# Kernel optimization log

Measured on AMD Instinct MI355X. Metric: run time of the kernel, lower is better.

## Reference

```python
import jax, jax.numpy as jnp
import numpy as np

B, S, D = 2, 2048, 1024
H, HKV, DK = 16, 4, 64          # n_heads, n_kv_heads, head dim
NREP = H // HKV                  # 4


def apply_rope(x):
    # Faithful to the original: positions run over x.shape[-2], which is the
    # HEAD axis (x is [B, S, H, DK]) due to how the torch module is written.
    d = x.shape[-1]
    h = x.shape[-2]
    inv_freq = 1.0 / (10000.0 ** (jnp.arange(0, d, 2, dtype=jnp.float32) / d))
    freqs = jnp.arange(h, dtype=jnp.float32)[:, None] * inv_freq[None, :]  # [H, DK/2]
    cos, sin = jnp.cos(freqs), jnp.sin(freqs)
    x1, x2 = x[..., 0::2], x[..., 1::2]
    # interleave back: stack on new last axis then flatten
    return jnp.stack([x1 * cos - x2 * sin, x1 * sin + x2 * cos], axis=-1).reshape(x.shape)


def setup_inputs() -> dict:
    key = jax.random.key(0)
    kx, kq, kk, kv, ko = jax.random.split(key, 5)
    std = 0.02
    x = jax.random.normal(kx, (B, S, D), jnp.float32)
    w_q = jax.random.normal(kq, (D, H * DK), jnp.float32) * std
    w_k = jax.random.normal(kk, (D, HKV * DK), jnp.float32) * std
    w_v = jax.random.normal(kv, (D, HKV * DK), jnp.float32) * std
    w_o = jax.random.normal(ko, (D, D), jnp.float32) * std
    # causal mask, broadcastable to [B, H, S, S]
    mask = jnp.tril(jnp.ones((S, S), bool))[None, None]  # [1,1,S,S]
    return {"x": x, "w_q": w_q, "w_k": w_k, "w_v": w_v, "w_o": w_o, "mask": mask}


def reference(x, w_q, w_k, w_v, w_o, mask):
    b, s, d = x.shape
    Q = (x @ w_q).reshape(b, s, H, DK)
    K = (x @ w_k).reshape(b, s, HKV, DK)
    V = (x @ w_v).reshape(b, s, HKV, DK)
    Q = apply_rope(Q)
    K = apply_rope(K)
    # [B,H,S,DK] with query heads grouped per kv head (matches repeat_interleave)
    Q = Q.transpose(0, 2, 1, 3).reshape(b, HKV, NREP, s, DK)
    K = K.transpose(0, 2, 1, 3)  # [B,HKV,S,DK]
    V = V.transpose(0, 2, 1, 3)
    scores = jnp.einsum('bgrqd,bgkd->bgrqk', Q, K) / np.float32(np.sqrt(DK))
    scores = scores.astype(jnp.float32)
    neg = jnp.finfo(jnp.float32).min
    scores = jnp.where(mask[:, :, None, :, :], scores, neg)  # [1,1,1,S,S] broadcast
    w = jax.nn.softmax(scores, axis=-1)
    ctx = jnp.einsum('bgrqk,bgkd->bgrqd', w, V)  # [B,HKV,NREP,S,DK]
    ctx = ctx.reshape(b, H, s, DK).transpose(0, 2, 1, 3).reshape(b, s, d)
    return ctx @ w_o
```

## Files before the change

### kernel.cpp

```cpp
#include <hip/hip_runtime.h>
#include <hip/hip_bf16.h>

#define S_LEN 2048
#define NBATCH 2
#define DMODEL 1024
#define NHEAD 16
#define NKV 4
#define HDIM 64

typedef __attribute__((ext_vector_type(4))) float f32x4;
typedef __attribute__((ext_vector_type(8))) short s16x8;

#define QSCALE 0.18033688011112042f

__device__ __forceinline__ unsigned short f32_bf16(float f) {
    unsigned int u = __float_as_uint(f);
    u += 0x7FFFu + ((u >> 16) & 1u);
    return (unsigned short)(u >> 16);
}

__device__ __forceinline__ unsigned int cvt_pk_bf16(float a, float b) {
    unsigned int r;
    asm("v_cvt_pk_bf16_f32 %0, %1, %2" : "=v"(r) : "v"(a), "v"(b));
    return r;
}

__device__ __forceinline__ void cvtT_body(const float* __restrict__ in,
                                          unsigned short* __restrict__ out,
                                          int N, int n_off, int bx, int by, int tid) {
    __shared__ float t[64][65];
    const int n0 = bx * 64;
    const int k0 = by * 64;
    const int r  = tid >> 4;
    const int c4 = (tid & 15) * 4;
    #pragma unroll
    for (int i = 0; i < 4; ++i) {
        const float4 v = *reinterpret_cast<const float4*>(
            in + (size_t)(k0 + i*16 + r) * N + n0 + c4);
        t[i*16 + r][c4+0] = v.x; t[i*16 + r][c4+1] = v.y;
        t[i*16 + r][c4+2] = v.z; t[i*16 + r][c4+3] = v.w;
    }
    __syncthreads();
    #pragma unroll
    for (int i = 0; i < 4; ++i) {
        const int n = i*16 + r;
        ushort4 o;
        o.x = f32_bf16(t[c4+0][n]); o.y = f32_bf16(t[c4+1][n]);
        o.z = f32_bf16(t[c4+2][n]); o.w = f32_bf16(t[c4+3][n]);
        *reinterpret_cast<ushort4*>(out + (size_t)(n_off + n0 + n) * 1024 + k0 + c4) = o;
    }
}

__global__ __launch_bounds__(256) void cvt_all_k(
    const float* __restrict__ x,  const float* __restrict__ wq,
    const float* __restrict__ wk, const float* __restrict__ wv,
    const float* __restrict__ wo,
    unsigned short* __restrict__ xb, unsigned short* __restrict__ Wqkvt,
    unsigned short* __restrict__ Wot)
{
    const int bid = blockIdx.x;
    if (bid < 4096) {
        const int i = bid * 256 + threadIdx.x;
        const float4 v = reinterpret_cast<const float4*>(x)[i];
        ushort4 r;
        r.x = f32_bf16(v.x); r.y = f32_bf16(v.y);
        r.z = f32_bf16(v.z); r.w = f32_bf16(v.w);
        reinterpret_cast<ushort4*>(xb)[i] = r;
    } else if (bid < 4480) {
        const int t  = bid - 4096;
        int bx = t % 24;
        const int by = t / 24;
        const float* in; int N, n_off;
        if (bx < 16)      { in = wq; N = 1024; n_off = 0; }
        else if (bx < 20) { in = wk; N = 256;  n_off = 1024; bx -= 16; }
        else              { in = wv; N = 256;  n_off = 1280; bx -= 20; }
        cvtT_body(in, Wqkvt, N, n_off, bx, by, threadIdx.x);
    } else {
        const int t = bid - 4480;
        cvtT_body(wo, Wot, 1024, 0, t % 16, t / 16, threadIdx.x);
    }
}

using gas_u32 = const unsigned int __attribute__((address_space(1))) *;
using las_u32 = unsigned int __attribute__((address_space(3))) *;

template<int EPI>
__global__ __launch_bounds__(256, 3) void gemm2_k(
    const unsigned short* __restrict__ A,
    const unsigned short* __restrict__ Bt,
    int N, int K,
    float* __restrict__ OutF,
    unsigned short* __restrict__ Qb,
    unsigned short* __restrict__ Kbuf,
    unsigned short* __restrict__ Vbuf)
{
    __shared__ unsigned short As[2][128 * 64];
    __shared__ unsigned short Bs[2][64 * 64];

    const int tid  = threadIdx.x;
    const int lane = tid & 63;
    const int l15  = lane & 15;
    const int l4   = lane >> 4;
    const int wave = tid >> 6;
    const int wm   = wave >> 1;
    const int wn   = wave & 1;
    const int bm   = blockIdx.y * 128;
    const int bn   = blockIdx.x * 64;

    f32x4 acc[4][2] = {};

    const int NT = K >> 6;

    #define GSTAGE(buf, k0)                                                        \
        {                                                                          \
            _Pragma("unroll")                                                      \
            for (int p = 0; p < 4; ++p) {                                          \
                const int c = p*256 + tid, r_ = c >> 3;                            \
                const int nc = (c & 7) ^ (r_ & 7);                                 \
                __builtin_amdgcn_global_load_lds(                                  \
                    (gas_u32)(A + (size_t)(bm + r_) * K + (k0) + nc*8),            \
                    (las_u32)(&As[buf][c*8]), 16, 0, 0);                           \
            }                                                                      \
            _Pragma("unroll")                                                      \
            for (int p = 0; p < 2; ++p) {                                          \
                const int c = p*256 + tid, r_ = c >> 3;                            \
                const int nc = (c & 7) ^ (r_ & 7);                                 \
                __builtin_amdgcn_global_load_lds(                                  \
                    (gas_u32)(Bt + (size_t)(bn + r_) * K + (k0) + nc*8),           \
                    (las_u32)(&Bs[buf][c*8]), 16, 0, 0);                           \
            }                                                                      \
        }

    GSTAGE(0, 0); __syncthreads();

    for (int kt = 0; kt < NT; ++kt) {
        const int cur = kt & 1;
        if (kt + 1 < NT) GSTAGE(cur ^ 1, (kt + 1) << 6);
        #pragma unroll
        for (int ks = 0; ks < 2; ++ks) {
            s16x8 af[4], bfv[2];
            #pragma unroll
            for (int mi = 0; mi < 4; ++mi) {
                const int r = wm*64 + mi*16 + l15;
                af[mi] = *reinterpret_cast<const s16x8*>(
                    &As[cur][r*64 + (((ks*4 + l4) ^ (r & 7)) * 8)]);
            }
            #pragma unroll
            for (int nj = 0; nj < 2; ++nj) {
                const int r = wn*32 + nj*16 + l15;
                bfv[nj] = *reinterpret_cast<const s16x8*>(
                    &Bs[cur][r*64 + (((ks*4 + l4) ^ (r & 7)) * 8)]);
            }
            #pragma unroll
            for (int mi = 0; mi < 4; ++mi)
                #pragma unroll
                for (int nj = 0; nj < 2; ++nj)
                    acc[mi][nj] = __builtin_amdgcn_mfma_f32_16x16x32_bf16(
                        af[mi], bfv[nj], acc[mi][nj], 0, 0, 0);
        }
        __syncthreads();
    }
    #undef GSTAGE

    #pragma unroll
    for (int mi = 0; mi < 4; ++mi) {
        #pragma unroll
        for (int nj = 0; nj < 2; ++nj) {
            #pragma unroll
            for (int v = 0; v < 4; ++v) {
                const int gr = bm + wm*64 + mi*16 + l4*4 + v;
                const int gc = bn + wn*32 + nj*16 + l15;
                float val = acc[mi][nj][v];
                if (EPI == 0) {
                    OutF[(size_t)gr * N + gc] = val;
                } else {
                    const int b  = gr >> 11;
                    const int sr = gr & (S_LEN - 1);
                    const int dk = gc & 63;
                    if (bn < 1024) {
                        const float partner = __shfl_xor(val, 1, 64);
                        const int   jp  = dk >> 1;
                        const float inv = __expf((float)jp * (-2.0f / 64.0f) * 9.210340371976184f);
                        const int   hh  = gc >> 6;
                        float sn, cs;
                        __sincosf((float)hh * inv, &sn, &cs);
                        val = ((gc & 1) == 0) ? (val * cs - partner * sn)
                                              : (partner * sn + val * cs);
                        val *= QSCALE;
                        Qb[(((size_t)b * NHEAD + hh) * S_LEN + sr) * HDIM + dk] = f32_bf16(val);
                    } else if (bn < 1280) {
                        const float partner = __shfl_xor(val, 1, 64);
                        const int   jp  = dk >> 1;
                        const float inv = __expf((float)jp * (-2.0f / 64.0f) * 9.210340371976184f);
                        const int   hh  = (gc - 1024) >> 6;
                        float sn, cs;
                        __sincosf((float)hh * inv, &sn, &cs);
                        val = ((gc & 1) == 0) ? (val * cs - partner * sn)
                                              : (partner * sn + val * cs);
                        Kbuf[(((size_t)b * NKV + hh) * S_LEN + sr) * HDIM + dk] = f32_bf16(val);
                    } else {
                        const int hh = (gc - 1280) >> 6;
                        Vbuf[(((size_t)b * NKV + hh) * HDIM + dk) * S_LEN + sr] = f32_bf16(val);
                    }
                }
            }
        }
    }
}


__device__ __forceinline__ void stage_load(
    const unsigned short* __restrict__ Kp,
    const unsigned short* __restrict__ Vp,
    int kv0, int tid, s16x8& kr, s16x8& vr)
{
    const int r = tid >> 3, col = (tid & 7) * 8;
    kr = *reinterpret_cast<const s16x8*>(Kp + (size_t)(kv0 + r) * HDIM + col);
    vr = *reinterpret_cast<const s16x8*>(Vp + (size_t)r * S_LEN + kv0 + col);
}

__device__ __forceinline__ void stage_write(
    unsigned short (*Ksb)[72], unsigned short (*Vsb)[72],
    int tid, const s16x8& kr, const s16x8& vr)
{
    const int r = tid >> 3, col = (tid & 7) * 8;
    *reinterpret_cast<s16x8*>(&Ksb[r][col]) = kr;
    *reinterpret_cast<s16x8*>(&Vsb[r][col]) = vr;
}

template<bool MASK>
__device__ __forceinline__ void attn_compute(
    int l15, int l4, int wloc,
    const unsigned short (*Ksb)[72], const unsigned short (*Vsb)[72],
    const s16x8 qf[2], f32x4 o[4], float& m, float& lsum,
    unsigned short (*Plds)[72])
{
    f32x4 s[4] = {};
    __builtin_amdgcn_s_setprio(1);
    #pragma unroll
    for (int c = 0; c < 4; ++c)
        #pragma unroll
        for (int ks = 0; ks < 2; ++ks) {
            const s16x8 kf = *reinterpret_cast<const s16x8*>(&Ksb[c*16 + l15][ks*32 + l4*8]);
            s[c] = __builtin_amdgcn_mfma_f32_16x16x32_bf16(kf, qf[ks], s[c], 0, 0, 0);
        }
    __builtin_amdgcn_s_setprio(0);

    if (MASK) {
        const int qloc = wloc + l15;
        #pragma unroll
        for (int c = 0; c < 4; ++c)
            #pragma unroll
            for (int v = 0; v < 4; ++v) {
                const int kvloc = c*16 + l4*4 + v;
                s[c][v] = (kvloc <= qloc) ? s[c][v] : -1e30f;
            }
    }

    float mc[4];
    #pragma unroll
    for (int c = 0; c < 4; ++c)
        mc[c] = fmaxf(fmaxf(s[c][0], s[c][1]), fmaxf(s[c][2], s[c][3]));
    float mx = fmaxf(fmaxf(mc[0], mc[1]), fmaxf(mc[2], mc[3]));
    if (!__all(mx <= m + 8.0f)) {
        mx = fmaxf(mx, __shfl_xor(mx, 16, 64));
        mx = fmaxf(mx, __shfl_xor(mx, 32, 64));
        const float mnew  = fmaxf(m, mx);
        const float scale = __builtin_amdgcn_exp2f(m - mnew);
        lsum *= scale;
        #pragma unroll
        for (int dkc = 0; dkc < 4; ++dkc) o[dkc] *= scale;
        m = mnew;
    }
    float psum = 0.0f;
    #pragma unroll
    for (int c = 0; c < 4; ++c)
        #pragma unroll
        for (int v = 0; v < 4; ++v) {
            const float p = __builtin_amdgcn_exp2f(s[c][v] - m);
            s[c][v] = p;
            psum += p;
        }
    lsum += psum;

    #pragma unroll
    for (int c = 0; c < 4; ++c) {
        uint2 w;
        w.x = cvt_pk_bf16(s[c][0], s[c][1]);
        w.y = cvt_pk_bf16(s[c][2], s[c][3]);
        *reinterpret_cast<uint2*>(&Plds[l15][c*16 + l4*4]) = w;
    }
    s16x8 pb[2];
    #pragma unroll
    for (int ks = 0; ks < 2; ++ks)
        pb[ks] = *reinterpret_cast<const s16x8*>(&Plds[l15][ks*32 + l4*8]);

    __builtin_amdgcn_s_setprio(1);
    #pragma unroll
    for (int dkc = 0; dkc < 4; ++dkc)
        #pragma unroll
        for (int ks = 0; ks < 2; ++ks) {
            const s16x8 vf = *reinterpret_cast<const s16x8*>(&Vsb[dkc*16 + l15][ks*32 + l4*8]);
            o[dkc] = __builtin_amdgcn_mfma_f32_16x16x32_bf16(vf, pb[ks], o[dkc], 0, 0, 0);
        }
    __builtin_amdgcn_s_setprio(0);
}

__global__ __launch_bounds__(512, 2) void attn_k(
    const unsigned short* __restrict__ Q,
    const unsigned short* __restrict__ Kb,
    const unsigned short* __restrict__ Vt,
    unsigned short* __restrict__ Ctx)
{
    __shared__ unsigned short Ks[2][64][72];
    __shared__ unsigned short Vs[2][64][72];
    __shared__ unsigned short Plds[8][16][72];

    const int tid  = threadIdx.x;
    const int lane = tid & 63;
    const int l15  = lane & 15;
    const int l4   = lane >> 4;
    const int wave = tid >> 6;

    const int L  = blockIdx.x;
    const int h  = L & 15;
    const int b  = (L >> 4) & 1;
    const int p  = (L >> 5) & 7;
    const int qt = (L < 256) ? (15 - p) : p;
    const int qb0 = qt * 128;

    const int g   = h >> 2;

    const unsigned short* Qp = Q  + ((size_t)b * NHEAD + h) * S_LEN * HDIM;
    const unsigned short* Kp = Kb + ((size_t)b * NKV  + g) * S_LEN * HDIM;
    const unsigned short* Vp = Vt + ((size_t)b * NKV  + g) * HDIM * S_LEN;

    const int qb = qb0 + wave * 16;
    const int dt = qb >> 6;
    const int NT = qt * 2 + 2;

    s16x8 qf[2];
    #pragma unroll
    for (int ks = 0; ks < 2; ++ks)
        qf[ks] = *reinterpret_cast<const s16x8*>(Qp + (size_t)(qb + l15) * HDIM + ks*32 + l4*8);

    f32x4 o[4] = {};
    float m = -1e30f, lsum = 0.0f;

    {
        s16x8 kr, vr;
        stage_load(Kp, Vp, 0, tid, kr, vr);
        stage_write(Ks[0], Vs[0], tid, kr, vr);
        __syncthreads();
    }

    for (int t = 0; t < NT; ++t) {
        const int cur = t & 1;
        s16x8 kr, vr;
        const bool more = (t + 1 < NT);
        if (more) stage_load(Kp, Vp, (t + 1) * 64, tid, kr, vr);
        if (t < dt)
            attn_compute<false>(l15, l4, wave*16 - t*64 + qb0, Ks[cur], Vs[cur], qf, o, m, lsum, Plds[wave]);
        else if (t == dt)
            attn_compute<true >(l15, l4, wave*16 - t*64 + qb0, Ks[cur], Vs[cur], qf, o, m, lsum, Plds[wave]);
        if (more) stage_write(Ks[cur ^ 1], Vs[cur ^ 1], tid, kr, vr);
        __syncthreads();
    }

    lsum += __shfl_xor(lsum, 16, 64);
    lsum += __shfl_xor(lsum, 32, 64);
    const float inv = 1.0f / lsum;
    unsigned short* cp = Ctx + (((size_t)b * S_LEN + qb + l15) * NHEAD + h) * HDIM;
    #pragma unroll
    for (int dkc = 0; dkc < 4; ++dkc) {
        uint2 r;
        r.x = cvt_pk_bf16(o[dkc][0] * inv, o[dkc][1] * inv);
        r.y = cvt_pk_bf16(o[dkc][2] * inv, o[dkc][3] * inv);
        *reinterpret_cast<uint2*>(cp + dkc*16 + l4*4) = r;
    }
}

extern "C" void kernel_launch(void* const* d_in, const int* in_sizes, int n_in,
                              void* d_out, int out_size, void* d_ws, size_t ws_size,
                              hipStream_t stream) {
    const float* x  = (const float*)d_in[0];
    const float* wq = (const float*)d_in[1];
    const float* wk = (const float*)d_in[2];
    const float* wv = (const float*)d_in[3];
    const float* wo = (const float*)d_in[4];
    float* out = (float*)d_out;

    const int M  = NBATCH * S_LEN;
    const int nX = M * DMODEL;
    const int nQ = NBATCH * NHEAD * S_LEN * HDIM;
    const int nKV = NBATCH * NKV * S_LEN * HDIM;

    unsigned short* xb    = (unsigned short*)d_ws;
    unsigned short* Wqkvt = xb + nX;
    unsigned short* Wot   = Wqkvt + 1536 * 1024;
    unsigned short* Qb    = Wot + 1024 * 1024;
    unsigned short* Kb    = Qb + nQ;
    unsigned short* Vbuf  = Kb + nKV;
    unsigned short* Ctx   = xb;

    cvt_all_k<<<dim3(4736), 256, 0, stream>>>(x, wq, wk, wv, wo, xb, Wqkvt, Wot);

    gemm2_k<1><<<dim3(1536/64, M/128), 256, 0, stream>>>(
        xb, Wqkvt, 1536, DMODEL, nullptr, Qb, Kb, Vbuf);

    attn_k<<<dim3(512, 1, 1), 512, 0, stream>>>(Qb, Kb, Vbuf, Ctx);

    gemm2_k<0><<<dim3(DMODEL/64, M/128), 256, 0, stream>>>(
        Ctx, Wot, DMODEL, DMODEL, out, nullptr, nullptr, nullptr);
}
```

Baseline: 91.94 us.

## Stream K/V tiles straight into LDS with XOR-swizzled unpadded layout

The attention kernel no longer stages K and V tiles through registers. It now issues global_load_lds so each tile goes from global memory directly into shared memory. The padded 72-wide LDS rows are replaced with dense 64-wide rows that use an XOR swizzle on 16-byte chunks, keyed by the row, to avoid bank conflicts on the MFMA fragment reads. This is meant to cut VGPR use and the register round-trip for prefetching. It relies on __syncthreads waiting for the outstanding async loads, and the swizzle must match between the writes and the reads.

```diff
diff --git a/kernel.cpp b/kernel.cpp
--- a/kernel.cpp
+++ b/kernel.cpp
@@ -209,39 +209,23 @@
 }
 
 
-__device__ __forceinline__ void stage_load(
-    const unsigned short* __restrict__ Kp,
-    const unsigned short* __restrict__ Vp,
-    int kv0, int tid, s16x8& kr, s16x8& vr)
-{
-    const int r = tid >> 3, col = (tid & 7) * 8;
-    kr = *reinterpret_cast<const s16x8*>(Kp + (size_t)(kv0 + r) * HDIM + col);
-    vr = *reinterpret_cast<const s16x8*>(Vp + (size_t)r * S_LEN + kv0 + col);
-}
-
-__device__ __forceinline__ void stage_write(
-    unsigned short (*Ksb)[72], unsigned short (*Vsb)[72],
-    int tid, const s16x8& kr, const s16x8& vr)
-{
-    const int r = tid >> 3, col = (tid & 7) * 8;
-    *reinterpret_cast<s16x8*>(&Ksb[r][col]) = kr;
-    *reinterpret_cast<s16x8*>(&Vsb[r][col]) = vr;
-}
-
 template<bool MASK>
 __device__ __forceinline__ void attn_compute(
     int l15, int l4, int wloc,
-    const unsigned short (*Ksb)[72], const unsigned short (*Vsb)[72],
+    const unsigned short* __restrict__ Ksb,
+    const unsigned short* __restrict__ Vsb,
     const s16x8 qf[2], f32x4 o[4], float& m, float& lsum,
     unsigned short (*Plds)[72])
 {
+    const int sw7 = l15 & 7;
     f32x4 s[4] = {};
     __builtin_amdgcn_s_setprio(1);
     #pragma unroll
     for (int c = 0; c < 4; ++c)
         #pragma unroll
         for (int ks = 0; ks < 2; ++ks) {
-            const s16x8 kf = *reinterpret_cast<const s16x8*>(&Ksb[c*16 + l15][ks*32 + l4*8]);
+            const s16x8 kf = *reinterpret_cast<const s16x8*>(
+                &Ksb[(c*16 + l15)*64 + (((ks*4 + l4) ^ sw7) * 8)]);
             s[c] = __builtin_amdgcn_mfma_f32_16x16x32_bf16(kf, qf[ks], s[c], 0, 0, 0);
         }
     __builtin_amdgcn_s_setprio(0);
@@ -300,7 +284,8 @@
     for (int dkc = 0; dkc < 4; ++dkc)
         #pragma unroll
         for (int ks = 0; ks < 2; ++ks) {
-            const s16x8 vf = *reinterpret_cast<const s16x8*>(&Vsb[dkc*16 + l15][ks*32 + l4*8]);
+            const s16x8 vf = *reinterpret_cast<const s16x8*>(
+                &Vsb[(dkc*16 + l15)*64 + (((ks*4 + l4) ^ sw7) * 8)]);
             o[dkc] = __builtin_amdgcn_mfma_f32_16x16x32_bf16(vf, pb[ks], o[dkc], 0, 0, 0);
         }
     __builtin_amdgcn_s_setprio(0);
@@ -312,8 +297,8 @@
     const unsigned short* __restrict__ Vt,
     unsigned short* __restrict__ Ctx)
 {
-    __shared__ unsigned short Ks[2][64][72];
-    __shared__ unsigned short Vs[2][64][72];
+    __shared__ unsigned short Ks[2][64 * 64];
+    __shared__ unsigned short Vs[2][64 * 64];
     __shared__ unsigned short Plds[8][16][72];
 
     const int tid  = threadIdx.x;
@@ -339,6 +324,18 @@
     const int dt = qb >> 6;
     const int NT = qt * 2 + 2;
 
+    #define AST(buf, kv0)                                                          \
+        {                                                                          \
+            const int r_ = tid >> 3, s_ = tid & 7;                                 \
+            const int nc = s_ ^ (r_ & 7);                                          \
+            __builtin_amdgcn_global_load_lds(                                      \
+                (gas_u32)(Kp + (size_t)((kv0) + r_) * HDIM + nc*8),                \
+                (las_u32)(&Ks[buf][tid*8]), 16, 0, 0);                             \
+            __builtin_amdgcn_global_load_lds(                                      \
+                (gas_u32)(Vp + (size_t)r_ * S_LEN + (kv0) + nc*8),                 \
+                (las_u32)(&Vs[buf][tid*8]), 16, 0, 0);                             \
+        }
+
     s16x8 qf[2];
     #pragma unroll
     for (int ks = 0; ks < 2; ++ks)
@@ -347,25 +344,19 @@
     f32x4 o[4] = {};
     float m = -1e30f, lsum = 0.0f;
 
-    {
-        s16x8 kr, vr;
-        stage_load(Kp, Vp, 0, tid, kr, vr);
-        stage_write(Ks[0], Vs[0], tid, kr, vr);
-        __syncthreads();
-    }
+    AST(0, 0);
+    __syncthreads();
 
     for (int t = 0; t < NT; ++t) {
         const int cur = t & 1;
-        s16x8 kr, vr;
-        const bool more = (t + 1 < NT);
-        if (more) stage_load(Kp, Vp, (t + 1) * 64, tid, kr, vr);
+        if (t + 1 < NT) AST(cur ^ 1, (t + 1) * 64);
         if (t < dt)
             attn_compute<false>(l15, l4, wave*16 - t*64 + qb0, Ks[cur], Vs[cur], qf, o, m, lsum, Plds[wave]);
         else if (t == dt)
             attn_compute<true >(l15, l4, wave*16 - t*64 + qb0, Ks[cur], Vs[cur], qf, o, m, lsum, Plds[wave]);
-        if (more) stage_write(Ks[cur ^ 1], Vs[cur ^ 1], tid, kr, vr);
         __syncthreads();
     }
+    #undef AST
 
     lsum += __shfl_xor(lsum, 16, 64);
     lsum += __shfl_xor(lsum, 32, 64);
```

Result: slower. 98.54 us (+7.2%).
